# Performance work log

Measured on AMD Instinct MI355X. Metric: run time of the kernel, lower is better.

## Reference

```python
import jax, jax.numpy as jnp
import numpy as np

B, N, C, D = 16, 2048, 256, 256


def setup_inputs() -> dict:
    key = jax.random.key(0)
    ks = jax.random.split(key, 8)
    x = jax.random.normal(ks[0], (B, N, C), dtype=jnp.float32)
    valid_len = jax.random.randint(ks[1], (B,), 0, N)
    # nn.Linear params: weight [out, in], bias [out]
    s = 1.0 / np.sqrt(C)
    Wq = jax.random.uniform(ks[2], (D, C), dtype=jnp.float32, minval=-s, maxval=s)
    bq = jax.random.uniform(ks[3], (D,), dtype=jnp.float32, minval=-s, maxval=s)
    Wk = jax.random.uniform(ks[4], (D, C), dtype=jnp.float32, minval=-s, maxval=s)
    bk = jax.random.uniform(ks[5], (D,), dtype=jnp.float32, minval=-s, maxval=s)
    Wv = jax.random.uniform(ks[6], (D, C), dtype=jnp.float32, minval=-s, maxval=s)
    bv = jax.random.uniform(ks[7], (D,), dtype=jnp.float32, minval=-s, maxval=s)
    return {"x": x, "valid_len": valid_len, "Wq": Wq, "bq": bq,
            "Wk": Wk, "bk": bk, "Wv": Wv, "bv": bv}


def reference(x, valid_len, Wq, bq, Wk, bk, Wv, bv):
    # QKV projections (nn.Linear: x @ W^T + b)
    q = jnp.einsum('bnc,dc->bnd', x, Wq) + bq
    k = jnp.einsum('bnc,dc->bnd', x, Wk) + bk
    v = jnp.einsum('bnc,dc->bnd', x, Wv) + bv
    # scores [B, N, N] = q @ k^T (no scaling: scale_factor_d unused in forward)
    scores = jnp.einsum('bnd,bmd->bnm', q, k)
    # key-side valid-length mask: arange(N) < valid_len[b], broadcast over queries
    mask = jnp.arange(N)[None, :] < valid_len[:, None]          # [B, N]
    scores = jnp.where(mask[:, None, :], scores, jnp.float32(-1000000.0))
    attn = jax.nn.softmax(scores, axis=-1)
    return jnp.einsum('bnm,bmd->bnd', attn, v)
```

## Files before the change

kernel.cpp:

```cpp
#include <hip/hip_runtime.h>
#include <hip/hip_bf16.h>
#include <stdint.h>

typedef __attribute__((ext_vector_type(8))) _Float16 half8;
typedef __attribute__((ext_vector_type(4))) _Float16 half4;
typedef __attribute__((ext_vector_type(2))) __fp16 fp16x2;
typedef __attribute__((ext_vector_type(4))) float f32x4;
typedef __attribute__((ext_vector_type(16))) float f32x16;
typedef __attribute__((ext_vector_type(4))) float float4v;

#define DEVI static __device__ __forceinline__

constexpr int Bb = 16, Nn = 2048, Cc = 256, Dd = 256;

DEVI unsigned short f2h_bits(float f) {
  _Float16 h = (_Float16)f;
  union { _Float16 h; unsigned short u; } c;
  c.h = h;
  return c.u;
}

DEVI void gl_lds16(const void* gsrc, void* ldst) {
  __builtin_amdgcn_global_load_lds(
      (const __attribute__((address_space(1))) unsigned int*)gsrc,
      (__attribute__((address_space(3))) unsigned int*)ldst, 16, 0, 0);
}

DEVI f32x4 mfma16h(half8 a, half8 b, f32x4 c) {
  return __builtin_amdgcn_mfma_f32_16x16x32_f16(a, b, c, 0, 0, 0);
}
DEVI f32x16 mfma32h(half8 a, half8 b, f32x16 c) {
  return __builtin_amdgcn_mfma_f32_32x32x16_f16(a, b, c, 0, 0, 0);
}

DEVI unsigned int pkrtz(float a, float b) {
  union { fp16x2 h; unsigned int u; } c;
  c.h = __builtin_amdgcn_cvt_pkrtz(a, b);
  return c.u;
}

__global__ void k_split_x(const float* __restrict__ x, _Float16* __restrict__ xh) {
  int i = blockIdx.x * 256 + threadIdx.x;
  float4v v = reinterpret_cast<const float4v*>(x)[i];
  half4 h;
#pragma unroll
  for (int j = 0; j < 4; ++j) h[j] = (_Float16)v[j];
  reinterpret_cast<half4*>(xh)[i] = h;
}

__global__ void k_split_w(const float* __restrict__ wq, const float* __restrict__ wk,
                          const float* __restrict__ wv, _Float16* __restrict__ wh) {
  int i = blockIdx.x * 256 + threadIdx.x;
  int mat = i >> 16;
  int rem = i & 65535;
  const float* w = (mat == 0) ? wq : ((mat == 1) ? wk : wv);
  wh[(size_t)mat * 65536 + rem] = (_Float16)w[rem];
}

__global__ __launch_bounds__(256, 2) void k_qkv(
    const _Float16* __restrict__ xh, const _Float16* __restrict__ wh,
    const float* __restrict__ bq, const float* __restrict__ bk, const float* __restrict__ bv,
    _Float16* __restrict__ qout, _Float16* __restrict__ kout, _Float16* __restrict__ vt) {
  __shared__ __align__(16) unsigned short smem[17408];

  const int tid = threadIdx.x;
  const int m0 = blockIdx.x * 128;
  const int n0 = blockIdx.y * 128;
  const int mat = blockIdx.z;
  const _Float16* wmat = wh + (size_t)mat * 65536;
  const int wave = tid >> 6, lane = tid & 63;
  const int wr = wave >> 1, wc = wave & 1;
  const int l15 = lane & 15, lq = lane >> 4;

  f32x4 zero4 = {0.f, 0.f, 0.f, 0.f};
  f32x4 acc[4][4];
#pragma unroll
  for (int a = 0; a < 4; ++a)
#pragma unroll
    for (int b2 = 0; b2 < 4; ++b2) acc[a][b2] = zero4;

  char* As = (char*)smem;
  char* Bs = (char*)smem + 16384;

  for (int kc = 0; kc < 4; ++kc) {
#pragma unroll
    for (int i = 0; i < 4; ++i) {
      int p = i * 4096 + tid * 16;
      int row = p >> 7;
      int src_in_row = (p & 127) ^ ((row & 7) << 4);
      const char* g = (const char*)(xh + (size_t)(m0 + row) * Cc + kc * 64) + src_in_row;
      gl_lds16(g, As + p);
    }
#pragma unroll
    for (int i = 0; i < 4; ++i) {
      int p = i * 4096 + tid * 16;
      int row = p >> 7;
      int src_in_row = (p & 127) ^ ((row & 7) << 4);
      const char* g = (const char*)(wmat + (size_t)(n0 + row) * Cc + kc * 64) + src_in_row;
      gl_lds16(g, Bs + p);
    }
    __syncthreads();
#pragma unroll
    for (int ks = 0; ks < 2; ++ks) {
      half8 af[4], bfr[4];
#pragma unroll
      for (int mf = 0; mf < 4; ++mf) {
        int row = wr * 64 + mf * 16 + l15;
        int byte = (row * 128 + ks * 64 + lq * 16) ^ ((row & 7) << 4);
        af[mf] = *(const half8*)(As + byte);
      }
#pragma unroll
      for (int nf = 0; nf < 4; ++nf) {
        int row = wc * 64 + nf * 16 + l15;
        int byte = (row * 128 + ks * 64 + lq * 16) ^ ((row & 7) << 4);
        bfr[nf] = *(const half8*)(Bs + byte);
      }
#pragma unroll
      for (int mf = 0; mf < 4; ++mf)
#pragma unroll
        for (int nf = 0; nf < 4; ++nf) acc[mf][nf] = mfma16h(af[mf], bfr[nf], acc[mf][nf]);
    }
    __syncthreads();
  }

  const float* bias = (mat == 0) ? bq : ((mat == 1) ? bk : bv);
  if (mat < 2) {
    _Float16* oo = (mat == 0) ? qout : kout;
#pragma unroll
    for (int nf = 0; nf < 4; ++nf) {
      int col = n0 + wc * 64 + nf * 16 + l15;
      float bval = bias[col];
#pragma unroll
      for (int mf = 0; mf < 4; ++mf) {
        int grow = m0 + wr * 64 + mf * 16 + lq * 4;
#pragma unroll
        for (int r = 0; r < 4; ++r)
          oo[(size_t)(grow + r) * Dd + col] = (_Float16)(acc[mf][nf][r] + bval);
      }
    }
  } else {
    __syncthreads();
#pragma unroll
    for (int nf = 0; nf < 4; ++nf) {
      int dl = wc * 64 + nf * 16 + l15;
      float bval = bias[n0 + dl];
#pragma unroll
      for (int mf = 0; mf < 4; ++mf) {
        int nl = wr * 64 + mf * 16 + lq * 4;
#pragma unroll
        for (int r = 0; r < 4; ++r) smem[dl * 136 + nl + r] = f2h_bits(acc[mf][nf][r] + bval);
      }
    }
    __syncthreads();
    const int bbat = m0 >> 11, tok0 = m0 & 2047;
#pragma unroll
    for (int pss = 0; pss < 8; ++pss) {
      int idx = pss * 256 + tid;
      int dl = idx >> 4;
      int cu = idx & 15;
      half8 vval = *(const half8*)((const char*)smem + dl * 272 + cu * 16);
      size_t off = ((size_t)bbat * Dd + n0 + dl) * Nn + tok0 + cu * 8;
      *(half8*)(vt + off) = vval;
    }
  }
}

__global__ __launch_bounds__(512, 2) void k_attn(
    const _Float16* __restrict__ qg, const _Float16* __restrict__ kin,
    const _Float16* __restrict__ vt, const int* __restrict__ vlen,
    float* __restrict__ out) {
  __shared__ __align__(16) char SMEM[149504];
  char* const KVb = SMEM;
  unsigned int* const PL = (unsigned int*)(SMEM + 131072);
  float* const mex = (float*)(SMEM + 147456);
  float* const lex = (float*)(SMEM + 148480);

  const int tid = threadIdx.x;
  const int wave = tid >> 6, lane = tid & 63;
  const int l31 = lane & 31, h = lane >> 5;
  const int wq = wave >> 1, wk = wave & 1;
  const int id = blockIdx.x;
  const int g = id & 7;
  const int j = id >> 3;
  const int b = g + 8 * (j >> 4);
  const int q0 = (j & 15) * 128;
  const int L = vlen[b];
  const bool uni = (L == 0);
  const int Lk = uni ? Nn : L;
  const int nt = (Lk + 63) >> 6;

  const char* kbase = (const char*)(kin + (size_t)b * Nn * Dd);
  const char* vbase = (const char*)(vt + (size_t)b * Dd * Nn);
  const char* qbase = (const char*)(qg + ((size_t)b * Nn + q0) * Dd);

  auto STAGE = [&](int buf, int t) {
    char* dst = KVb + buf * 65536;
    const int k0 = t * 64;
#pragma unroll
    for (int i = 0; i < 4; ++i) {
      int p = i * 8192 + tid * 16;
      int row = p >> 9;
      int sl = ((p & 511) >> 4) ^ (row & 31);
      gl_lds16(kbase + (size_t)(k0 + row) * 512 + (sl << 4), dst + p);
    }
#pragma unroll
    for (int i = 0; i < 4; ++i) {
      int p = i * 8192 + tid * 16;
      int r = p >> 9;
      int sl = ((p & 511) >> 4) ^ (r & 31);
      int cl = sl << 4;
      int d = r * 4 + (cl >> 7);
      int kbyte = cl & 127;
      gl_lds16(vbase + (size_t)d * (Nn * 2) + (size_t)k0 * 2 + kbyte, dst + 32768 + p);
    }
  };

  STAGE(0, 0);
#pragma unroll
  for (int i = 0; i < 8; ++i) {
    int p = i * 8192 + tid * 16;
    int row = p >> 9;
    int sl = ((p & 511) >> 4) ^ (row & 31);
    gl_lds16(qbase + (size_t)row * 512 + (sl << 4), KVb + 65536 + p);
  }
  asm volatile("s_waitcnt vmcnt(0)" ::: "memory");
  asm volatile("s_barrier" ::: "memory");

  half8 qreg[16];
  {
    const int row = wq * 32 + l31;
#pragma unroll
    for (int kt = 0; kt < 16; ++kt) {
      int byte = row * 512 + (((kt * 2 + h) ^ (row & 31)) << 4);
      qreg[kt] = *(const half8*)(KVb + 65536 + byte);
    }
  }
  asm volatile("s_waitcnt lgkmcnt(0)" ::: "memory");
  asm volatile("s_barrier" ::: "memory");

  f32x16 acc[4];
#pragma unroll
  for (int dg = 0; dg < 4; ++dg)
#pragma unroll
    for (int r = 0; r < 16; ++r) acc[dg][r] = 0.f;
  float m = -__builtin_inff();
  float lsum = 0.f;

  for (int t = 0; t < nt; ++t) {
    const int cur = t & 1;
    if (t + 1 < nt) {
      STAGE(cur ^ 1, t + 1);
      asm volatile("s_waitcnt vmcnt(8)" ::: "memory");
    } else {
      asm volatile("s_waitcnt vmcnt(0)" ::: "memory");
    }
    asm volatile("s_barrier" ::: "memory");

    const char* Ks = KVb + cur * 65536;
    const char* Vs = Ks + 32768;
    const int k0 = t * 64;

    f32x16 st;
#pragma unroll
    for (int r = 0; r < 16; ++r) st[r] = 0.f;
    if (!uni) {
      const int key = wk * 32 + l31;
      __builtin_amdgcn_s_setprio(1);
#pragma unroll
      for (int kt = 0; kt < 16; ++kt) {
        int byte = key * 512 + (((kt * 2 + h) ^ l31) << 4);
        half8 kf = *(const half8*)(Ks + byte);
        st = mfma32h(kf, qreg[kt], st);
      }
      __builtin_amdgcn_s_setprio(0);
      if (k0 + 64 > L) {
#pragma unroll
        for (int r = 0; r < 16; ++r) {
          int keyg = k0 + wk * 32 + (r & 3) + 8 * (r >> 2) + 4 * h;
          if (keyg >= L) st[r] = -1e6f;
        }
      }
    }

    float pm = st[0];
#pragma unroll
    for (int r = 1; r < 16; ++r) pm = fmaxf(pm, st[r]);
    pm = fmaxf(pm, __shfl_xor(pm, 32));
    if (lane < 32) mex[wave * 32 + lane] = pm;
    asm volatile("s_waitcnt lgkmcnt(0)\ns_barrier" ::: "memory");
    float pmo = mex[(wave ^ 1) * 32 + l31];
    float mnew = fmaxf(m, fmaxf(pm, pmo));
    float scale = __expf(m - mnew);
    m = mnew;
    float psum = 0.f;
#pragma unroll
    for (int r = 0; r < 16; ++r) {
      float p_ = __expf(st[r] - mnew);
      st[r] = p_;
      psum += p_;
    }
    lsum = lsum * scale + psum;

#pragma unroll
    for (int i = 0; i < 8; ++i) {
      unsigned int pk = pkrtz(st[2 * i], st[2 * i + 1]);
      int kp = wk * 16 + 4 * (i >> 1) + (i & 1) + 2 * h;
      PL[wq * 1024 + kp * 32 + l31] = pk;
    }
    asm volatile("s_waitcnt lgkmcnt(0)\ns_barrier" ::: "memory");

    union { unsigned int u[4]; half8 v; } pf0, pf1, pf2, pf3;
#pragma unroll
    for (int w = 0; w < 4; ++w) {
      pf0.u[w] = PL[wq * 1024 + (0 * 8 + h * 4 + w) * 32 + l31];
      pf1.u[w] = PL[wq * 1024 + (1 * 8 + h * 4 + w) * 32 + l31];
      pf2.u[w] = PL[wq * 1024 + (2 * 8 + h * 4 + w) * 32 + l31];
      pf3.u[w] = PL[wq * 1024 + (3 * 8 + h * 4 + w) * 32 + l31];
    }

#pragma unroll
    for (int dg = 0; dg < 4; ++dg)
#pragma unroll
      for (int r = 0; r < 16; ++r) acc[dg][r] *= scale;

    __builtin_amdgcn_s_setprio(1);
#pragma unroll
    for (int dg = 0; dg < 4; ++dg) {
      int r = wk * 32 + dg * 8 + (l31 >> 2);
#pragma unroll
      for (int ks = 0; ks < 4; ++ks) {
        int slot = (l31 & 3) * 8 + ks * 2 + h;
        half8 vf = *(const half8*)(Vs + r * 512 + ((slot ^ (r & 31)) << 4));
        acc[dg] = mfma32h(vf, ks == 0 ? pf0.v : (ks == 1 ? pf1.v : (ks == 2 ? pf2.v : pf3.v)),
                          acc[dg]);
      }
    }
    __builtin_amdgcn_s_setprio(0);

    asm volatile("s_barrier" ::: "memory");
  }

  lsum += __shfl_xor(lsum, 32);
  if (lane < 32) lex[wave * 32 + lane] = lsum;
  asm volatile("s_waitcnt lgkmcnt(0)\ns_barrier" ::: "memory");
  float linv = 1.f / (lsum + lex[(wave ^ 1) * 32 + l31]);

  float* T = (float*)SMEM;
  {
    const int ql = wq * 32 + l31;
#pragma unroll
    for (int dg = 0; dg < 4; ++dg)
#pragma unroll
      for (int r = 0; r < 16; ++r) {
        int d = wk * 128 + dg * 32 + (r & 3) + 8 * (r >> 2) + 4 * h;
        T[ql * 260 + d] = acc[dg][r] * linv;
      }
  }
  asm volatile("s_waitcnt lgkmcnt(0)\ns_barrier" ::: "memory");

  {
    const int rb = tid >> 6;
    const int c4 = (tid & 63) * 4;
#pragma unroll
    for (int i = 0; i < 16; ++i) {
      int row = rb + i * 8;
      float4v v = *(const float4v*)(T + row * 260 + c4);
      *(float4v*)(out + ((size_t)b * Nn + q0 + row) * Dd + c4) = v;
    }
  }
}

extern "C" void kernel_launch(void* const* d_in, const int* in_sizes, int n_in,
                              void* d_out, int out_size, void* d_ws, size_t ws_size,
                              hipStream_t stream) {
  const float* x = (const float*)d_in[0];
  const int* vlen = (const int*)d_in[1];
  const float* Wq = (const float*)d_in[2];
  const float* bq = (const float*)d_in[3];
  const float* Wk = (const float*)d_in[4];
  const float* bk = (const float*)d_in[5];
  const float* Wv = (const float*)d_in[6];
  const float* bv = (const float*)d_in[7];
  float* out = (float*)d_out;
  char* ws = (char*)d_ws;

  _Float16* qh = (_Float16*)(ws);
  _Float16* kk = (_Float16*)(ws + 16777216);
  _Float16* vt = (_Float16*)(ws + 33554432);
  _Float16* wh = (_Float16*)(ws + 50331648);
  _Float16* xh = (_Float16*)d_out;

  k_split_x<<<8192, 256, 0, stream>>>(x, xh);
  k_split_w<<<768, 256, 0, stream>>>(Wq, Wk, Wv, wh);
  k_qkv<<<dim3(256, 2, 3), 256, 0, stream>>>(xh, wh, bq, bk, bv, qh, kk, vt);
  k_attn<<<256, 512, 0, stream>>>(qh, kk, vt, vlen, out);
}
```

Before: 118.2 us.

## Load V tiles straight to registers from tiled layout, shrink LDS, defer max sync

The projection kernel now writes V^T in per-64-token tiles laid out so each wave can load its MFMA V operands directly from global memory into registers, rather than staging V through LDS. LDS use falls from about 146KB to about 82KB, which may allow more blocks per CU. The per-tile softmax now uses each wave's local max and sum, and the two key-halves are merged after the existing barrier by rescaling the fp16 P fragments. This removes one barrier per tile. The output writeback is split into two phases to fit the smaller LDS. It risks global-load latency on V and some fp16 rescaling precision loss.

```diff
diff --git a/kernel.cpp b/kernel.cpp
--- a/kernel.cpp
+++ b/kernel.cpp
@@ -159,7 +159,8 @@
       int dl = idx >> 4;
       int cu = idx & 15;
       half8 vval = *(const half8*)((const char*)smem + dl * 272 + cu * 16);
-      size_t off = ((size_t)bbat * Dd + n0 + dl) * Nn + tok0 + cu * 8;
+      int tt = (tok0 >> 6) + (cu >> 3);
+      size_t off = (((size_t)bbat * 32 + tt) * 256 + (n0 + dl)) * 64 + (cu & 7) * 8;
       *(half8*)(vt + off) = vval;
     }
   }
@@ -169,11 +170,10 @@
     const _Float16* __restrict__ qg, const _Float16* __restrict__ kin,
     const _Float16* __restrict__ vt, const int* __restrict__ vlen,
     float* __restrict__ out) {
-  __shared__ __align__(16) char SMEM[149504];
-  char* const KVb = SMEM;
-  unsigned int* const PL = (unsigned int*)(SMEM + 131072);
-  float* const mex = (float*)(SMEM + 147456);
-  float* const lex = (float*)(SMEM + 148480);
+  __shared__ __align__(16) char SMEM[83968];
+  char* const Kb = SMEM;
+  unsigned int* const PL = (unsigned int*)(SMEM + 65536);
+  float* const MLX = (float*)(SMEM + 81920);
 
   const int tid = threadIdx.x;
   const int wave = tid >> 6, lane = tid & 63;
@@ -190,53 +190,42 @@
   const int nt = (Lk + 63) >> 6;
 
   const char* kbase = (const char*)(kin + (size_t)b * Nn * Dd);
-  const char* vbase = (const char*)(vt + (size_t)b * Dd * Nn);
+  const _Float16* vtile = vt + (size_t)b * 32 * 256 * 64;
   const char* qbase = (const char*)(qg + ((size_t)b * Nn + q0) * Dd);
 
-  auto STAGE = [&](int buf, int t) {
-    char* dst = KVb + buf * 65536;
-    const int k0 = t * 64;
+  auto STAGEK = [&](int buf, int t) {
+    char* dst = Kb + buf * 32768;
+    const int k0t = t * 64;
 #pragma unroll
     for (int i = 0; i < 4; ++i) {
       int p = i * 8192 + tid * 16;
       int row = p >> 9;
       int sl = ((p & 511) >> 4) ^ (row & 31);
-      gl_lds16(kbase + (size_t)(k0 + row) * 512 + (sl << 4), dst + p);
-    }
-#pragma unroll
-    for (int i = 0; i < 4; ++i) {
-      int p = i * 8192 + tid * 16;
-      int r = p >> 9;
-      int sl = ((p & 511) >> 4) ^ (r & 31);
-      int cl = sl << 4;
-      int d = r * 4 + (cl >> 7);
-      int kbyte = cl & 127;
-      gl_lds16(vbase + (size_t)d * (Nn * 2) + (size_t)k0 * 2 + kbyte, dst + 32768 + p);
+      gl_lds16(kbase + (size_t)(k0t + row) * 512 + (sl << 4), dst + p);
     }
   };
 
-  STAGE(0, 0);
 #pragma unroll
   for (int i = 0; i < 8; ++i) {
     int p = i * 8192 + tid * 16;
     int row = p >> 9;
     int sl = ((p & 511) >> 4) ^ (row & 31);
-    gl_lds16(qbase + (size_t)row * 512 + (sl << 4), KVb + 65536 + p);
+    gl_lds16(qbase + (size_t)row * 512 + (sl << 4), Kb + p);
   }
   asm volatile("s_waitcnt vmcnt(0)" ::: "memory");
   asm volatile("s_barrier" ::: "memory");
-
   half8 qreg[16];
   {
     const int row = wq * 32 + l31;
 #pragma unroll
     for (int kt = 0; kt < 16; ++kt) {
       int byte = row * 512 + (((kt * 2 + h) ^ (row & 31)) << 4);
-      qreg[kt] = *(const half8*)(KVb + 65536 + byte);
+      qreg[kt] = *(const half8*)(Kb + byte);
     }
   }
   asm volatile("s_waitcnt lgkmcnt(0)" ::: "memory");
   asm volatile("s_barrier" ::: "memory");
+  STAGEK(0, 0);
 
   f32x16 acc[4];
 #pragma unroll
@@ -248,16 +237,25 @@
 
   for (int t = 0; t < nt; ++t) {
     const int cur = t & 1;
+    const _Float16* vt_t = vtile + (size_t)t * (256 * 64);
+
+    half8 vA[8];
+#pragma unroll
+    for (int dg = 0; dg < 2; ++dg)
+#pragma unroll
+      for (int ks = 0; ks < 4; ++ks)
+        vA[dg * 4 + ks] =
+            *(const half8*)(vt_t + (size_t)(wk * 128 + dg * 32 + l31) * 64 + ks * 16 + h * 8);
+
     if (t + 1 < nt) {
-      STAGE(cur ^ 1, t + 1);
+      STAGEK(cur ^ 1, t + 1);
+      asm volatile("s_waitcnt vmcnt(12)" ::: "memory");
+    } else {
       asm volatile("s_waitcnt vmcnt(8)" ::: "memory");
-    } else {
-      asm volatile("s_waitcnt vmcnt(0)" ::: "memory");
     }
     asm volatile("s_barrier" ::: "memory");
 
-    const char* Ks = KVb + cur * 65536;
-    const char* Vs = Ks + 32768;
+    const char* Ks = Kb + cur * 32768;
     const int k0 = t * 64;
 
     f32x16 st;
@@ -286,20 +284,14 @@
 #pragma unroll
     for (int r = 1; r < 16; ++r) pm = fmaxf(pm, st[r]);
     pm = fmaxf(pm, __shfl_xor(pm, 32));
-    if (lane < 32) mex[wave * 32 + lane] = pm;
-    asm volatile("s_waitcnt lgkmcnt(0)\ns_barrier" ::: "memory");
-    float pmo = mex[(wave ^ 1) * 32 + l31];
-    float mnew = fmaxf(m, fmaxf(pm, pmo));
-    float scale = __expf(m - mnew);
-    m = mnew;
     float psum = 0.f;
 #pragma unroll
     for (int r = 0; r < 16; ++r) {
-      float p_ = __expf(st[r] - mnew);
+      float p_ = __expf(st[r] - pm);
       st[r] = p_;
       psum += p_;
     }
-    lsum = lsum * scale + psum;
+    psum += __shfl_xor(psum, 32);
 
 #pragma unroll
     for (int i = 0; i < 8; ++i) {
@@ -307,7 +299,30 @@
       int kp = wk * 16 + 4 * (i >> 1) + (i & 1) + 2 * h;
       PL[wq * 1024 + kp * 32 + l31] = pk;
     }
+    if (h == 0) {
+      MLX[((wq * 2 + wk) * 2 + 0) * 32 + l31] = pm;
+      MLX[((wq * 2 + wk) * 2 + 1) * 32 + l31] = psum;
+    }
+
+    half8 vB[8];
+#pragma unroll
+    for (int dg = 0; dg < 2; ++dg)
+#pragma unroll
+      for (int ks = 0; ks < 4; ++ks)
+        vB[dg * 4 + ks] =
+            *(const half8*)(vt_t + (size_t)(wk * 128 + (dg + 2) * 32 + l31) * 64 + ks * 16 + h * 8);
+
     asm volatile("s_waitcnt lgkmcnt(0)\ns_barrier" ::: "memory");
+
+    float pm0 = MLX[((wq * 2 + 0) * 2 + 0) * 32 + l31];
+    float ps0 = MLX[((wq * 2 + 0) * 2 + 1) * 32 + l31];
+    float pm1 = MLX[((wq * 2 + 1) * 2 + 0) * 32 + l31];
+    float ps1 = MLX[((wq * 2 + 1) * 2 + 1) * 32 + l31];
+    float mnew = fmaxf(m, fmaxf(pm0, pm1));
+    float scale = __expf(m - mnew);
+    m = mnew;
+    float s0 = __expf(pm0 - mnew), s1 = __expf(pm1 - mnew);
+    lsum = lsum * scale + s0 * ps0 + s1 * ps1;
 
     union { unsigned int u[4]; half8 v; } pf0, pf1, pf2, pf3;
 #pragma unroll
@@ -317,6 +332,15 @@
       pf2.u[w] = PL[wq * 1024 + (2 * 8 + h * 4 + w) * 32 + l31];
       pf3.u[w] = PL[wq * 1024 + (3 * 8 + h * 4 + w) * 32 + l31];
     }
+    {
+      _Float16 s0h = (_Float16)s0, s1h = (_Float16)s1;
+      half8 sc0 = {s0h, s0h, s0h, s0h, s0h, s0h, s0h, s0h};
+      half8 sc1 = {s1h, s1h, s1h, s1h, s1h, s1h, s1h, s1h};
+      pf0.v *= sc0;
+      pf1.v *= sc0;
+      pf2.v *= sc1;
+      pf3.v *= sc1;
+    }
 
 #pragma unroll
     for (int dg = 0; dg < 4; ++dg)
@@ -326,46 +350,42 @@
     __builtin_amdgcn_s_setprio(1);
 #pragma unroll
     for (int dg = 0; dg < 4; ++dg) {
-      int r = wk * 32 + dg * 8 + (l31 >> 2);
-#pragma unroll
-      for (int ks = 0; ks < 4; ++ks) {
-        int slot = (l31 & 3) * 8 + ks * 2 + h;
-        half8 vf = *(const half8*)(Vs + r * 512 + ((slot ^ (r & 31)) << 4));
-        acc[dg] = mfma32h(vf, ks == 0 ? pf0.v : (ks == 1 ? pf1.v : (ks == 2 ? pf2.v : pf3.v)),
-                          acc[dg]);
-      }
+      half8 v0 = (dg < 2) ? vA[dg * 4 + 0] : vB[(dg - 2) * 4 + 0];
+      half8 v1 = (dg < 2) ? vA[dg * 4 + 1] : vB[(dg - 2) * 4 + 1];
+      half8 v2 = (dg < 2) ? vA[dg * 4 + 2] : vB[(dg - 2) * 4 + 2];
+      half8 v3 = (dg < 2) ? vA[dg * 4 + 3] : vB[(dg - 2) * 4 + 3];
+      acc[dg] = mfma32h(v0, pf0.v, acc[dg]);
+      acc[dg] = mfma32h(v1, pf1.v, acc[dg]);
+      acc[dg] = mfma32h(v2, pf2.v, acc[dg]);
+      acc[dg] = mfma32h(v3, pf3.v, acc[dg]);
     }
     __builtin_amdgcn_s_setprio(0);
 
     asm volatile("s_barrier" ::: "memory");
   }
 
-  lsum += __shfl_xor(lsum, 32);
-  if (lane < 32) lex[wave * 32 + lane] = lsum;
-  asm volatile("s_waitcnt lgkmcnt(0)\ns_barrier" ::: "memory");
-  float linv = 1.f / (lsum + lex[(wave ^ 1) * 32 + l31]);
-
+  float linv = 1.f / lsum;
   float* T = (float*)SMEM;
-  {
-    const int ql = wq * 32 + l31;
-#pragma unroll
-    for (int dg = 0; dg < 4; ++dg)
-#pragma unroll
-      for (int r = 0; r < 16; ++r) {
-        int d = wk * 128 + dg * 32 + (r & 3) + 8 * (r >> 2) + 4 * h;
-        T[ql * 260 + d] = acc[dg][r] * linv;
-      }
-  }
-  asm volatile("s_waitcnt lgkmcnt(0)\ns_barrier" ::: "memory");
-
-  {
-    const int rb = tid >> 6;
-    const int c4 = (tid & 63) * 4;
-#pragma unroll
-    for (int i = 0; i < 16; ++i) {
+#pragma unroll
+  for (int ph = 0; ph < 2; ++ph) {
+    __syncthreads();
+    if ((wq >> 1) == ph) {
+      int ql = (wq & 1) * 32 + l31;
+#pragma unroll
+      for (int dg = 0; dg < 4; ++dg)
+#pragma unroll
+        for (int r = 0; r < 16; ++r) {
+          int d = wk * 128 + dg * 32 + (r & 3) + 8 * (r >> 2) + 4 * h;
+          T[ql * 260 + d] = acc[dg][r] * linv;
+        }
+    }
+    __syncthreads();
+    const int rb = tid >> 6, c4 = (tid & 63) * 4;
+#pragma unroll
+    for (int i = 0; i < 8; ++i) {
       int row = rb + i * 8;
       float4v v = *(const float4v*)(T + row * 260 + c4);
-      *(float4v*)(out + ((size_t)b * Nn + q0 + row) * Dd + c4) = v;
+      *(float4v*)(out + ((size_t)b * Nn + q0 + ph * 64 + row) * Dd + c4) = v;
     }
   }
 }
```

Result: slower. 202.6 us (+71.3%).

## Merge softmax max exchange into P barrier with local max and fp16 rescale

Applied to the files above, without the earlier changes.

Each wave now computes exponentials against its own local row max. It publishes its max and partial sum alongside the P tile, so the separate LDS barrier for exchanging maxima is removed. Each wave then rescales its P fragments in fp16 by exp(local-global max) before the PV MFMAs. The change also splits the QK^T MFMA chain into two independent accumulators and prefetches half the V fragments before the softmax. Scaling P in fp16 after truncating to fp16 may add precision loss or underflow when the local and global maxima differ widely.

```diff
diff --git a/kernel.cpp b/kernel.cpp
--- a/kernel.cpp
+++ b/kernel.cpp
@@ -172,8 +172,7 @@
   __shared__ __align__(16) char SMEM[149504];
   char* const KVb = SMEM;
   unsigned int* const PL = (unsigned int*)(SMEM + 131072);
-  float* const mex = (float*)(SMEM + 147456);
-  float* const lex = (float*)(SMEM + 148480);
+  float* const MLX = (float*)(SMEM + 147456);
 
   const int tid = threadIdx.x;
   const int wave = tid >> 6, lane = tid & 63;
@@ -261,18 +260,26 @@
     const int k0 = t * 64;
 
     f32x16 st;
-#pragma unroll
-    for (int r = 0; r < 16; ++r) st[r] = 0.f;
     if (!uni) {
       const int key = wk * 32 + l31;
+      f32x16 e0, e1;
+#pragma unroll
+      for (int r = 0; r < 16; ++r) {
+        e0[r] = 0.f;
+        e1[r] = 0.f;
+      }
       __builtin_amdgcn_s_setprio(1);
 #pragma unroll
-      for (int kt = 0; kt < 16; ++kt) {
-        int byte = key * 512 + (((kt * 2 + h) ^ l31) << 4);
-        half8 kf = *(const half8*)(Ks + byte);
-        st = mfma32h(kf, qreg[kt], st);
+      for (int kt = 0; kt < 16; kt += 2) {
+        int byteA = key * 512 + (((kt * 2 + h) ^ l31) << 4);
+        int byteB = key * 512 + ((((kt + 1) * 2 + h) ^ l31) << 4);
+        half8 kfA = *(const half8*)(Ks + byteA);
+        half8 kfB = *(const half8*)(Ks + byteB);
+        e0 = mfma32h(kfA, qreg[kt], e0);
+        e1 = mfma32h(kfB, qreg[kt + 1], e1);
       }
       __builtin_amdgcn_s_setprio(0);
+      st = e0 + e1;
       if (k0 + 64 > L) {
 #pragma unroll
         for (int r = 0; r < 16; ++r) {
@@ -280,26 +287,34 @@
           if (keyg >= L) st[r] = -1e6f;
         }
       }
+    } else {
+#pragma unroll
+      for (int r = 0; r < 16; ++r) st[r] = 0.f;
+    }
+
+    half8 vA[8];
+#pragma unroll
+    for (int dg = 0; dg < 2; ++dg) {
+      int r = wk * 32 + dg * 8 + (l31 >> 2);
+#pragma unroll
+      for (int ks = 0; ks < 4; ++ks) {
+        int slot = (l31 & 3) * 8 + ks * 2 + h;
+        vA[dg * 4 + ks] = *(const half8*)(Vs + r * 512 + ((slot ^ (r & 31)) << 4));
+      }
     }
 
     float pm = st[0];
 #pragma unroll
     for (int r = 1; r < 16; ++r) pm = fmaxf(pm, st[r]);
     pm = fmaxf(pm, __shfl_xor(pm, 32));
-    if (lane < 32) mex[wave * 32 + lane] = pm;
-    asm volatile("s_waitcnt lgkmcnt(0)\ns_barrier" ::: "memory");
-    float pmo = mex[(wave ^ 1) * 32 + l31];
-    float mnew = fmaxf(m, fmaxf(pm, pmo));
-    float scale = __expf(m - mnew);
-    m = mnew;
     float psum = 0.f;
 #pragma unroll
     for (int r = 0; r < 16; ++r) {
-      float p_ = __expf(st[r] - mnew);
+      float p_ = __expf(st[r] - pm);
       st[r] = p_;
       psum += p_;
     }
-    lsum = lsum * scale + psum;
+    psum += __shfl_xor(psum, 32);
 
 #pragma unroll
     for (int i = 0; i < 8; ++i) {
@@ -307,7 +322,21 @@
       int kp = wk * 16 + 4 * (i >> 1) + (i & 1) + 2 * h;
       PL[wq * 1024 + kp * 32 + l31] = pk;
     }
+    if (h == 0) {
+      MLX[((wq * 2 + wk) * 2 + 0) * 32 + l31] = pm;
+      MLX[((wq * 2 + wk) * 2 + 1) * 32 + l31] = psum;
+    }
     asm volatile("s_waitcnt lgkmcnt(0)\ns_barrier" ::: "memory");
+
+    float pm0 = MLX[((wq * 2 + 0) * 2 + 0) * 32 + l31];
+    float ps0 = MLX[((wq * 2 + 0) * 2 + 1) * 32 + l31];
+    float pm1 = MLX[((wq * 2 + 1) * 2 + 0) * 32 + l31];
+    float ps1 = MLX[((wq * 2 + 1) * 2 + 1) * 32 + l31];
+    float mnew = fmaxf(m, fmaxf(pm0, pm1));
+    float scale = __expf(m - mnew);
+    m = mnew;
+    float s0 = __expf(pm0 - mnew), s1 = __expf(pm1 - mnew);
+    lsum = lsum * scale + s0 * ps0 + s1 * ps1;
 
     union { unsigned int u[4]; half8 v; } pf0, pf1, pf2, pf3;
 #pragma unroll
@@ -317,6 +346,15 @@
       pf2.u[w] = PL[wq * 1024 + (2 * 8 + h * 4 + w) * 32 + l31];
       pf3.u[w] = PL[wq * 1024 + (3 * 8 + h * 4 + w) * 32 + l31];
     }
+    {
+      _Float16 s0h = (_Float16)s0, s1h = (_Float16)s1;
+      half8 sc0 = {s0h, s0h, s0h, s0h, s0h, s0h, s0h, s0h};
+      half8 sc1 = {s1h, s1h, s1h, s1h, s1h, s1h, s1h, s1h};
+      pf0.v *= sc0;
+      pf1.v *= sc0;
+      pf2.v *= sc1;
+      pf3.v *= sc1;
+    }
 
 #pragma unroll
     for (int dg = 0; dg < 4; ++dg)
@@ -326,24 +364,34 @@
     __builtin_amdgcn_s_setprio(1);
 #pragma unroll
     for (int dg = 0; dg < 4; ++dg) {
-      int r = wk * 32 + dg * 8 + (l31 >> 2);
-#pragma unroll
-      for (int ks = 0; ks < 4; ++ks) {
-        int slot = (l31 & 3) * 8 + ks * 2 + h;
-        half8 vf = *(const half8*)(Vs + r * 512 + ((slot ^ (r & 31)) << 4));
-        acc[dg] = mfma32h(vf, ks == 0 ? pf0.v : (ks == 1 ? pf1.v : (ks == 2 ? pf2.v : pf3.v)),
-                          acc[dg]);
-      }
+      half8 v0, v1, v2, v3;
+      if (dg < 2) {
+        v0 = vA[dg * 4 + 0];
+        v1 = vA[dg * 4 + 1];
+        v2 = vA[dg * 4 + 2];
+        v3 = vA[dg * 4 + 3];
+      } else {
+        int r = wk * 32 + dg * 8 + (l31 >> 2);
+        int s0l = (l31 & 3) * 8 + 0 * 2 + h;
+        int s1l = (l31 & 3) * 8 + 1 * 2 + h;
+        int s2l = (l31 & 3) * 8 + 2 * 2 + h;
+        int s3l = (l31 & 3) * 8 + 3 * 2 + h;
+        v0 = *(const half8*)(Vs + r * 512 + ((s0l ^ (r & 31)) << 4));
+        v1 = *(const half8*)(Vs + r * 512 + ((s1l ^ (r & 31)) << 4));
+        v2 = *(const half8*)(Vs + r * 512 + ((s2l ^ (r & 31)) << 4));
+        v3 = *(const half8*)(Vs + r * 512 + ((s3l ^ (r & 31)) << 4));
+      }
+      acc[dg] = mfma32h(v0, pf0.v, acc[dg]);
+      acc[dg] = mfma32h(v1, pf1.v, acc[dg]);
+      acc[dg] = mfma32h(v2, pf2.v, acc[dg]);
+      acc[dg] = mfma32h(v3, pf3.v, acc[dg]);
     }
     __builtin_amdgcn_s_setprio(0);
 
     asm volatile("s_barrier" ::: "memory");
   }
 
-  lsum += __shfl_xor(lsum, 32);
-  if (lane < 32) lex[wave * 32 + lane] = lsum;
-  asm volatile("s_waitcnt lgkmcnt(0)\ns_barrier" ::: "memory");
-  float linv = 1.f / (lsum + lex[(wave ^ 1) * 32 + l31]);
+  float linv = 1.f / lsum;
 
   float* T = (float*)SMEM;
   {
```

Result: slower. 126.7 us (+7.1%).
